# Kernel tuning notes

Measured on AMD Instinct MI355X. Metric: run time of the kernel, lower is better.

Reference implementation:

```python
import jax, jax.numpy as jnp
import numpy as np

B = 4096      # batch
N = 32768     # total tree nodes (real + pseudo classes) = columns of x
L = 12        # tree path depth (levels)
K = 64        # siblings (brother nodes) per level, padded to fixed width
C = 16384     # number of real classes (range of y)


def setup_inputs() -> dict:
    key = jax.random.key(0)
    k1, k2, k3, k4 = jax.random.split(key, 4)
    x = jax.random.normal(k1, (B, N), dtype=jnp.float32)
    # per-level sibling index sets (constants derived from the cover tree /
    # new2index / index2brother dicts in the original module)
    brother = jax.random.randint(k2, (L, K), 0, N)
    # the true path node at each level must be one of that level's siblings
    pos = jax.random.randint(k3, (L,), 0, K)
    p_y = brother[jnp.arange(L), pos]
    y = jax.random.randint(k4, (B,), 0, C)  # class labels (path selection baked into brother/p_y)
    return {"x": x, "brother": brother, "p_y": p_y, "y": y}


def reference(x, brother, p_y, y):
    # x: [B, N] logits over all tree nodes; brother: [L, K]; p_y: [L]
    gathered = x[:, brother]                      # [B, L, K] irregular column gather
    logp = jax.nn.log_softmax(gathered, axis=-1)  # per-level softmax over siblings
    # label = first position of the path node within its sibling set (torch nonzero()[0])
    labels = jnp.argmax(brother == p_y[:, None], axis=-1)          # [L]
    sel = jnp.take_along_axis(logp, labels[None, :, None], axis=2)[..., 0]  # [B, L]
    # CrossEntropyLoss = mean over batch of NLL, summed across tree levels
    return (-sel).mean(axis=0).sum()
```

## Files before the change

kernel.cpp:

```cpp
#include <hip/hip_runtime.h>

#define BB 4096
#define NN 32768
#define LL 12
#define KK 64

constexpr int WAVES_PER_BLOCK = 4;
constexpr int NBLOCKS = (BB * LL) / WAVES_PER_BLOCK;

__global__ __launch_bounds__(256) void hsm_partial(
    const float* __restrict__ x,
    const int* __restrict__ brother,
    const int* __restrict__ p_y,
    float* __restrict__ partials) {

    const int wave_in_block = threadIdx.x >> 6;
    const int lane = threadIdx.x & 63;
    const int waves_total = gridDim.x * WAVES_PER_BLOCK;
    const int wave_id = blockIdx.x * WAVES_PER_BLOCK + wave_in_block;
    const int total = BB * LL;

    float local = 0.f;
    for (int t = wave_id; t < total; t += waves_total) {
        const int b = t / LL;
        const int l = t - b * LL;
        const int idx = brother[l * KK + lane];
        const float v = x[(size_t)b * NN + idx];

        const unsigned long long m = __ballot(idx == p_y[l]);
        const int label = __ffsll(m) - 1;

        float mx = v;
        #pragma unroll
        for (int o = 32; o > 0; o >>= 1) mx = fmaxf(mx, __shfl_xor(mx, o));
        float s = __expf(v - mx);
        #pragma unroll
        for (int o = 32; o > 0; o >>= 1) s += __shfl_xor(s, o);
        const float lse = mx + __logf(s);

        const float vsel = __shfl(v, label);
        local += (lse - vsel);
    }

    __shared__ float red[WAVES_PER_BLOCK];
    if (lane == 0) red[wave_in_block] = local;
    __syncthreads();
    if (threadIdx.x == 0) {
        float s = 0.f;
        #pragma unroll
        for (int i = 0; i < WAVES_PER_BLOCK; ++i) s += red[i];
        partials[blockIdx.x] = s;
    }
}

__global__ __launch_bounds__(256) void hsm_final(
    const float* __restrict__ partials, float* __restrict__ out, int n) {
    float s = 0.f;
    for (int i = threadIdx.x; i < n; i += 256) s += partials[i];
    #pragma unroll
    for (int o = 32; o > 0; o >>= 1) s += __shfl_xor(s, o);
    __shared__ float red[4];
    const int wave = threadIdx.x >> 6, lane = threadIdx.x & 63;
    if (lane == 0) red[wave] = s;
    __syncthreads();
    if (threadIdx.x == 0) {
        out[0] = (red[0] + red[1] + red[2] + red[3]) / (float)BB;
    }
}

extern "C" void kernel_launch(void* const* d_in, const int* in_sizes, int n_in,
                              void* d_out, int out_size, void* d_ws, size_t ws_size,
                              hipStream_t stream) {
    const float* x       = (const float*)d_in[0];
    const int*   brother = (const int*)d_in[1];
    const int*   p_y     = (const int*)d_in[2];
    float* out      = (float*)d_out;
    float* partials = (float*)d_ws;

    hsm_partial<<<NBLOCKS, 256, 0, stream>>>(x, brother, p_y, partials);
    hsm_final<<<1, 256, 0, stream>>>(partials, out, NBLOCKS);
}
```

Measured before the change: 641.3 us.

## Process eight batch rows per wave with hoisted sibling index and label

Each wave now handles one tree level over a chunk of eight batch rows instead of one (row, level) pair. The sibling indices, target node and label ballot are loaded once per wave, and the eight gathered loads are issued together so more memory requests are in flight before the reductions. The grid shrinks eightfold, which reduces per-wave setup and the number of partials to sum, at the cost of more registers and fewer waves to hide latency.

Result: no change. 636.6 us (-0.7%).

```diff
diff --git a/kernel.cpp b/kernel.cpp
--- a/kernel.cpp
+++ b/kernel.cpp
@@ -5,8 +5,10 @@
 #define LL 12
 #define KK 64
 
-constexpr int WAVES_PER_BLOCK = 4;
-constexpr int NBLOCKS = (BB * LL) / WAVES_PER_BLOCK;
+constexpr int CHUNK = 8;
+constexpr int NWAVES = LL * (BB / CHUNK);
+constexpr int WPB = 4;
+constexpr int NBLOCKS = NWAVES / WPB;
 
 __global__ __launch_bounds__(256) void hsm_partial(
     const float* __restrict__ x,
@@ -16,39 +18,43 @@
 
     const int wave_in_block = threadIdx.x >> 6;
     const int lane = threadIdx.x & 63;
-    const int waves_total = gridDim.x * WAVES_PER_BLOCK;
-    const int wave_id = blockIdx.x * WAVES_PER_BLOCK + wave_in_block;
-    const int total = BB * LL;
+    const int wid = blockIdx.x * WPB + wave_in_block;
+
+    const int chunk = wid / LL;
+    const int l = wid - chunk * LL;
+    const int b0 = chunk * CHUNK;
+
+    const int col = brother[l * KK + lane];
+    const int py = p_y[l];
+    const int label = __ffsll(__ballot(col == py)) - 1;
+
+    const float* __restrict__ xp = x + (size_t)b0 * NN + col;
+
+    float v[CHUNK];
+    #pragma unroll
+    for (int bi = 0; bi < CHUNK; ++bi)
+        v[bi] = xp[(size_t)bi * NN];
 
     float local = 0.f;
-    for (int t = wave_id; t < total; t += waves_total) {
-        const int b = t / LL;
-        const int l = t - b * LL;
-        const int idx = brother[l * KK + lane];
-        const float v = x[(size_t)b * NN + idx];
-
-        const unsigned long long m = __ballot(idx == p_y[l]);
-        const int label = __ffsll(m) - 1;
-
-        float mx = v;
+    #pragma unroll
+    for (int bi = 0; bi < CHUNK; ++bi) {
+        float mx = v[bi];
         #pragma unroll
         for (int o = 32; o > 0; o >>= 1) mx = fmaxf(mx, __shfl_xor(mx, o));
-        float s = __expf(v - mx);
+        float s = __expf(v[bi] - mx);
         #pragma unroll
         for (int o = 32; o > 0; o >>= 1) s += __shfl_xor(s, o);
         const float lse = mx + __logf(s);
-
-        const float vsel = __shfl(v, label);
-        local += (lse - vsel);
+        local += lse - __shfl(v[bi], label);
     }
 
-    __shared__ float red[WAVES_PER_BLOCK];
+    __shared__ float red[WPB];
     if (lane == 0) red[wave_in_block] = local;
     __syncthreads();
     if (threadIdx.x == 0) {
         float s = 0.f;
         #pragma unroll
-        for (int i = 0; i < WAVES_PER_BLOCK; ++i) s += red[i];
+        for (int i = 0; i < WPB; ++i) s += red[i];
         partials[blockIdx.x] = s;
     }
 }
```
